# Optimization experiments

Hardware: AMD Instinct MI355X
Metric: run time of the kernel (lower is better)

Reference implementation:

```python
import jax, jax.numpy as jnp
import numpy as np

HIDDEN = 4096
NUM_HEADS = 32
NUM_KV_HEADS = 8
HEAD_DIM = HIDDEN // NUM_HEADS  # 128
ROPE_THETA = 500000.0
WORLD_SIZE = 4  # number of ring blocks (simulated single-device)


def setup_inputs() -> dict:
    key = jax.random.key(0)
    ks = jax.random.split(key, 5)
    B, S = 1, 2048
    wscale = HIDDEN ** -0.5  # keep activations O(1)
    return {
        "hidden_states": jax.random.normal(ks[0], (B, S, HIDDEN), jnp.float32),
        "position_ids": jnp.broadcast_to(jnp.arange(S, dtype=jnp.int32), (B, S)),
        "q_proj": jax.random.normal(ks[1], (NUM_HEADS * HEAD_DIM, HIDDEN), jnp.float32) * wscale,
        "k_proj": jax.random.normal(ks[2], (NUM_KV_HEADS * HEAD_DIM, HIDDEN), jnp.float32) * wscale,
        "v_proj": jax.random.normal(ks[3], (NUM_KV_HEADS * HEAD_DIM, HIDDEN), jnp.float32) * wscale,
        "o_proj": jax.random.normal(ks[4], (HIDDEN, NUM_HEADS * HEAD_DIM), jnp.float32) * wscale,
    }


def _rope_cos_sin(position_ids):
    # LlamaRotaryEmbedding: inv_freq over even dims, emb = cat(freqs, freqs)
    inv_freq = 1.0 / (ROPE_THETA ** (jnp.arange(0, HEAD_DIM, 2, dtype=jnp.float32) / HEAD_DIM))
    freqs = position_ids.astype(jnp.float32)[..., None] * inv_freq  # [B,S,HD/2]
    emb = jnp.concatenate([freqs, freqs], axis=-1)                  # [B,S,HD]
    return jnp.cos(emb), jnp.sin(emb)


def _rotate_half(x):
    x1, x2 = jnp.split(x, 2, axis=-1)
    return jnp.concatenate([-x2, x1], axis=-1)


def _attention_forward(hidden_states, q_proj, k_proj, v_proj, o_proj, position_ids):
    B, S, _ = hidden_states.shape
    # projections (no bias), layout [B, S, H, D] as in the source (view before RoPE)
    q = (hidden_states @ q_proj.T).reshape(B, S, NUM_HEADS, HEAD_DIM)
    k = (hidden_states @ k_proj.T).reshape(B, S, NUM_KV_HEADS, HEAD_DIM)
    v = (hidden_states @ v_proj.T).reshape(B, S, NUM_KV_HEADS, HEAD_DIM)

    cos, sin = _rope_cos_sin(position_ids)        # [B,S,HD]
    c, s = cos[:, :, None, :], sin[:, :, None, :]  # unsqueeze_dim=2
    q = q * c + _rotate_half(q) * s
    k = k * c + _rotate_half(k) * s

    # GQA: expand KV heads to match query heads
    groups = NUM_HEADS // NUM_KV_HEADS
    k = jnp.repeat(k, groups, axis=2)  # [B,S,NH,HD]
    v = jnp.repeat(v, groups, axis=2)

    sm_scale = HEAD_DIM ** -0.5
    blk = S // WORLD_SIZE

    # ring: per-KV-block partial attention (non-causal, as no mask is passed) + LSE
    outs, lses = [], []
    for w in range(WORLD_SIZE):
        kb = k[:, w * blk:(w + 1) * blk]
        vb = v[:, w * blk:(w + 1) * blk]
        scores = jnp.einsum('bqhd,bkhd->bhqk', q, kb) * sm_scale  # [B,NH,S,blk]
        m = jnp.max(scores, axis=-1, keepdims=True)
        p = jnp.exp(scores - m)
        l = jnp.sum(p, axis=-1, keepdims=True)
        outs.append(jnp.einsum('bhqk,bkhd->bqhd', p / l, vb))      # normalized partial out
        lses.append((m + jnp.log(l))[..., 0])                      # [B,NH,S]

    # merge_attentions: weight each block by exp(lse_b - logsumexp(lse))
    lse_all = jnp.stack(lses, axis=0)                 # [W,B,NH,S]
    wgt = jax.nn.softmax(lse_all, axis=0)
    attn = sum(outs[w] * jnp.transpose(wgt[w], (0, 2, 1))[..., None]
               for w in range(WORLD_SIZE))            # [B,S,NH,HD]

    attn = attn.reshape(B, S, NUM_HEADS * HEAD_DIM)
    return attn @ o_proj.T


def reference(hidden_states, position_ids, q_proj, k_proj, v_proj, o_proj):
    return _attention_forward(hidden_states, q_proj, k_proj, v_proj, o_proj, position_ids)
```

## Files before the change

### kernel.cpp

```cpp
#include <hip/hip_runtime.h>
#include <stdint.h>
#include <cmath>

typedef unsigned short u16;
typedef unsigned int u32;
typedef __attribute__((ext_vector_type(8))) __bf16 bf16x8;
typedef __attribute__((ext_vector_type(4))) float f32x4;

#define HIDDEN 4096
#define NH 32
#define NKV 8
#define HD 128
#define S_LEN 2048

__device__ __forceinline__ u16 f2bf(float f) {
    u32 x = __float_as_uint(f);
    x += 0x7fff + ((x >> 16) & 1);
    return (u16)(x >> 16);
}
__device__ __forceinline__ float bf2f(u16 u) {
    return __uint_as_float(((u32)u) << 16);
}
__device__ __forceinline__ float fexp2(float x) {
#if __has_builtin(__builtin_amdgcn_exp2f)
    return __builtin_amdgcn_exp2f(x);
#else
    return __expf(x * 0.6931471805599453f);
#endif
}

typedef __attribute__((address_space(1))) const void gv_t;
typedef __attribute__((address_space(3))) void lv_t;
__device__ __forceinline__ void async16(const u16* g, u16* s) {
    __builtin_amdgcn_global_load_lds((gv_t*)g, (lv_t*)s, 16, 0, 0);
}

#define F4_HS   2097152u
#define F4_WQ   4194304u
#define F4_WKV  1048576u
__global__ void cvt_all(const float* __restrict__ s0, const float* __restrict__ s1,
                        const float* __restrict__ s2, const float* __restrict__ s3,
                        const float* __restrict__ s4, u16* __restrict__ dst) {
    u32 i = blockIdx.x * 256 + threadIdx.x;
    const float* src; u32 off;
    if (i < F4_HS)                              { src = s0; off = 0; }
    else if (i < F4_HS + F4_WQ)                 { src = s1; off = F4_HS; }
    else if (i < F4_HS + F4_WQ + F4_WKV)        { src = s2; off = F4_HS + F4_WQ; }
    else if (i < F4_HS + F4_WQ + 2 * F4_WKV)    { src = s3; off = F4_HS + F4_WQ + F4_WKV; }
    else                                        { src = s4; off = F4_HS + F4_WQ + 2 * F4_WKV; }
    float4 v = ((const float4*)src)[i - off];
    union { u16 u[4]; uint2 w; } pk;
    pk.u[0] = f2bf(v.x); pk.u[1] = f2bf(v.y);
    pk.u[2] = f2bf(v.z); pk.u[3] = f2bf(v.w);
    ((uint2*)dst)[i] = pk.w;
}

#define GEMM_PROLOGUE_AND_MAINLOOP(Aptr, Bptr, Kdim)                                   \
    __shared__ u16 sMem[2][128 * 64];                                                  \
    u16* const sA = sMem[0];                                                           \
    u16* const sB = sMem[1];                                                           \
    const int tid = threadIdx.x;                                                       \
    const int w = tid >> 6, lane = tid & 63;                                           \
    const int l15 = lane & 15, quad = lane >> 4;                                       \
    const int m0 = blockIdx.y * 128, n0 = blockIdx.x * 128;                            \
    const int wm = w & 1, wn = w >> 1;                                                 \
    f32x4 acc[4][4];                                                                   \
    _Pragma("unroll") for (int mi = 0; mi < 4; ++mi)                                   \
    _Pragma("unroll") for (int ni = 0; ni < 4; ++ni)                                   \
    _Pragma("unroll") for (int r = 0; r < 4; ++r) acc[mi][ni][r] = 0.f;                \
    for (int kt = 0; kt < (Kdim); kt += 64) {                                          \
        _Pragma("unroll") for (int i = 0; i < 4; ++i) {                                \
            int c = (i * 4 + w) * 64 + lane;                                           \
            int r = c >> 3, sl = c & 7, g = sl ^ (r & 7);                              \
            async16((Aptr) + (size_t)(m0 + r) * (Kdim) + kt + g * 8, &sA[c * 8]);      \
        }                                                                              \
        _Pragma("unroll") for (int i = 0; i < 4; ++i) {                                \
            int c = (i * 4 + w) * 64 + lane;                                           \
            int r = c >> 3, sl = c & 7, g = sl ^ (r & 7);                              \
            async16((Bptr) + (size_t)(n0 + r) * (Kdim) + kt + g * 8, &sB[c * 8]);      \
        }                                                                              \
        __syncthreads();                                                               \
        _Pragma("unroll") for (int ks = 0; ks < 2; ++ks) {                             \
            bf16x8 af[4], bf[4];                                                       \
            _Pragma("unroll") for (int t = 0; t < 4; ++t) {                            \
                int row = wm * 64 + t * 16 + l15;                                      \
                int sl = (ks * 4 + quad) ^ (row & 7);                                  \
                af[t] = *(const bf16x8*)&sA[row * 64 + sl * 8];                        \
            }                                                                          \
            _Pragma("unroll") for (int t = 0; t < 4; ++t) {                            \
                int row = wn * 64 + t * 16 + l15;                                      \
                int sl = (ks * 4 + quad) ^ (row & 7);                                  \
                bf[t] = *(const bf16x8*)&sB[row * 64 + sl * 8];                        \
            }                                                                          \
            _Pragma("unroll") for (int mi = 0; mi < 4; ++mi)                           \
            _Pragma("unroll") for (int ni = 0; ni < 4; ++ni)                           \
                acc[mi][ni] = __builtin_amdgcn_mfma_f32_16x16x32_bf16(                 \
                    af[mi], bf[ni], acc[mi][ni], 0, 0, 0);                             \
        }                                                                              \
        __syncthreads();                                                               \
    }

__global__ __launch_bounds__(256, 2) void gemm_bt_f32(
    const u16* __restrict__ A, const u16* __restrict__ B, float* __restrict__ C,
    int N, int K)
{
    GEMM_PROLOGUE_AND_MAINLOOP(A, B, K)
#pragma unroll
    for (int mi = 0; mi < 4; ++mi) {
        int row = m0 + wm * 64 + mi * 16 + quad * 4;
#pragma unroll
        for (int ni = 0; ni < 4; ++ni) {
            int col = n0 + wn * 64 + ni * 16 + l15;
#pragma unroll
            for (int r = 0; r < 4; ++r)
                C[(size_t)(row + r) * N + col] = acc[mi][ni][r];
        }
    }
}

__global__ __launch_bounds__(256, 2) void gemm_qkv(
    const u16* __restrict__ A, const u16* __restrict__ B,
    u16* __restrict__ qb, u16* __restrict__ kbuf, u16* __restrict__ vt,
    const float2* __restrict__ tab)
{
    GEMM_PROLOGUE_AND_MAINLOOP(A, B, HIDDEN)
    if (n0 < 4096) {
#pragma unroll
        for (int mi = 0; mi < 4; ++mi) {
            int row = m0 + wm * 64 + mi * 16 + quad * 4;
#pragma unroll
            for (int ni = 0; ni < 4; ++ni) {
                int col = n0 + wn * 64 + ni * 16 + l15;
#pragma unroll
                for (int r = 0; r < 4; ++r)
                    qb[(size_t)(row + r) * HIDDEN + col] = f2bf(acc[mi][ni][r]);
            }
        }
    } else if (n0 < 4096 + 1024) {
        u16* const sT = (u16*)sMem;
        int cb = n0 - 4096;
#pragma unroll
        for (int mi = 0; mi < 4; ++mi)
#pragma unroll
            for (int ni = 0; ni < 4; ++ni) {
                int cl = wn * 64 + ni * 16 + l15;
#pragma unroll
                for (int r = 0; r < 4; ++r) {
                    int rl = wm * 64 + mi * 16 + quad * 4 + r;
                    sT[rl * 128 + cl] = f2bf(acc[mi][ni][r]);
                }
            }
        __syncthreads();
#pragma unroll
        for (int mi = 0; mi < 4; ++mi)
#pragma unroll
            for (int ni = 0; ni < 4; ++ni) {
                int cl = wn * 64 + ni * 16 + l15;
#pragma unroll
                for (int r = 0; r < 4; ++r) {
                    int rl = wm * 64 + mi * 16 + quad * 4 + r;
                    int srow = m0 + rl;
                    float x1 = bf2f(sT[rl * 128 + cl]);
                    float x2 = bf2f(sT[rl * 128 + (cl ^ 64)]);
                    float2 cs = tab[(size_t)srow * 64 + (cl & 63)];
                    float o = (cl < 64) ? (x1 * cs.x - x2 * cs.y)
                                        : (x1 * cs.x + x2 * cs.y);
                    kbuf[(size_t)srow * (NKV * HD) + cb + cl] = f2bf(o);
                }
            }
    } else {
        int cb = n0 - (4096 + 1024);
#pragma unroll
        for (int mi = 0; mi < 4; ++mi) {
            int row = m0 + wm * 64 + mi * 16 + quad * 4;
#pragma unroll
            for (int ni = 0; ni < 4; ++ni) {
                int c = cb + wn * 64 + ni * 16 + l15;
                union { u16 u[4]; uint2 v; } pk;
#pragma unroll
                for (int r = 0; r < 4; ++r) pk.u[r] = f2bf(acc[mi][ni][r]);
                *(uint2*)&vt[(size_t)c * S_LEN + row] = pk.v;
            }
        }
    }
}

struct DTab { double f[64]; };
__global__ void rope_table(const int* __restrict__ pos, float2* __restrict__ tab,
                           DTab dt) {
    int idx = blockIdx.x * 256 + threadIdx.x;
    int d = idx & 63, s = idx >> 6;
    double fr = (double)pos[s] * dt.f[d];
    double sd, cd;
    sincos(fr, &sd, &cd);
    tab[idx] = make_float2((float)cd, (float)sd);
}

__global__ __launch_bounds__(256, 2) void attn_kernel(
    const u16* __restrict__ Q, const u16* __restrict__ Kb,
    const u16* __restrict__ Vt, u16* __restrict__ O,
    const float2* __restrict__ tab, float qscale)
{
    __shared__ u16 sK[2][64 * 128];
    __shared__ u16 sV[2][128 * 64];

    const int tid = threadIdx.x;
    const int w = tid >> 6, lane = tid & 63;
    const int l15 = lane & 15, quad = lane >> 4;
    const int h = blockIdx.y, q0 = blockIdx.x * 128;
    const int hk = h >> 2;

    bf16x8 qf[2][4];
#pragma unroll
    for (int mt = 0; mt < 2; ++mt) {
        int srow = q0 + w * 32 + mt * 16 + l15;
        const u16* qrow = Q + (size_t)srow * HIDDEN + h * HD;
        bf16x8 raw[4];
#pragma unroll
        for (int ks = 0; ks < 4; ++ks)
            raw[ks] = *(const bf16x8*)(qrow + ks * 32 + quad * 8);
#pragma unroll
        for (int a = 0; a < 2; ++a) {
            const float2* tp = &tab[(size_t)srow * 64 + a * 32 + quad * 8];
#pragma unroll
            for (int j = 0; j < 8; ++j) {
                float c = tp[j].x * qscale, sn = tp[j].y * qscale;
                float x1 = (float)raw[a][j], x2 = (float)raw[a + 2][j];
                qf[mt][a][j]     = (__bf16)(x1 * c - x2 * sn);
                qf[mt][a + 2][j] = (__bf16)(x2 * c + x1 * sn);
            }
        }
    }

    f32x4 oc[8][2];
#pragma unroll
    for (int dt = 0; dt < 8; ++dt)
#pragma unroll
        for (int nt = 0; nt < 2; ++nt)
#pragma unroll
            for (int r = 0; r < 4; ++r) oc[dt][nt][r] = 0.f;
    float m_r[2], l_r[2];
#pragma unroll
    for (int mt = 0; mt < 2; ++mt) { m_r[mt] = -1e30f; l_r[mt] = 0.f; }

    auto stageK = [&](int k0, u16* dst) {
#pragma unroll
        for (int i = 0; i < 4; ++i) {
            int c = i * 256 + tid;
            int r = c >> 4, sl = c & 15, g = sl ^ (r & 15);
            async16(Kb + (size_t)(k0 + r) * (NKV * HD) + hk * HD + g * 8, &dst[c * 8]);
        }
    };
    auto stageV = [&](int k0, u16* dst) {
#pragma unroll
        for (int i = 0; i < 4; ++i) {
            int c = i * 256 + tid;
            int r = c >> 3, sl = c & 7, g = sl ^ (r & 7);
            async16(Vt + (size_t)(hk * HD + r) * S_LEN + k0 + g * 8, &dst[c * 8]);
        }
    };

    stageK(0, sK[0]);
    stageV(0, sV[0]);
    __syncthreads();

    int cur = 0;
    for (int kbi = 0; kbi < 32; ++kbi) {
        if (kbi < 31) {
            stageK((kbi + 1) * 64, sK[cur ^ 1]);
            stageV((kbi + 1) * 64, sV[cur ^ 1]);
        }
        const u16* sKc = sK[cur];
        const u16* sVc = sV[cur];

        f32x4 sa[4][2];
#pragma unroll
        for (int nt = 0; nt < 4; ++nt)
#pragma unroll
            for (int mt = 0; mt < 2; ++mt)
#pragma unroll
                for (int r = 0; r < 4; ++r) sa[nt][mt][r] = 0.f;
#pragma unroll
        for (int ks = 0; ks < 4; ++ks) {
            bf16x8 kf[4];
#pragma unroll
            for (int nt = 0; nt < 4; ++nt) {
                int row = nt * 16 + l15;
                int sl = (ks * 4 + quad) ^ (row & 15);
                kf[nt] = *(const bf16x8*)&sKc[row * 128 + sl * 8];
            }
#pragma unroll
            for (int nt = 0; nt < 4; ++nt)
#pragma unroll
                for (int mt = 0; mt < 2; ++mt)
                    sa[nt][mt] = __builtin_amdgcn_mfma_f32_16x16x32_bf16(
                        kf[nt], qf[mt][ks], sa[nt][mt], 0, 0, 0);
        }

        float mxv[2];
        bool grow = false;
#pragma unroll
        for (int mt = 0; mt < 2; ++mt) {
            float mx = sa[0][mt][0];
#pragma unroll
            for (int nt = 0; nt < 4; ++nt)
#pragma unroll
                for (int r = 0; r < 4; ++r)
                    if (nt || r) mx = fmaxf(mx, sa[nt][mt][r]);
            mx = fmaxf(mx, __shfl_xor(mx, 16));
            mx = fmaxf(mx, __shfl_xor(mx, 32));
            mxv[mt] = mx;
            grow = grow || (mx > m_r[mt] + 8.f);
        }
        const int dorescale = __any((int)grow);
        if (dorescale) {
            float al[2];
#pragma unroll
            for (int mt = 0; mt < 2; ++mt) {
                float mnew = fmaxf(m_r[mt], mxv[mt]);
                al[mt] = fexp2(m_r[mt] - mnew);
                m_r[mt] = mnew;
                l_r[mt] *= al[mt];
            }
#pragma unroll
            for (int dt = 0; dt < 8; ++dt)
#pragma unroll
                for (int r = 0; r < 4; ++r) { oc[dt][0][r] *= al[0]; oc[dt][1][r] *= al[1]; }
        }

        bf16x8 pf[2][2];
#pragma unroll
        for (int mt = 0; mt < 2; ++mt) {
            float mm = m_r[mt];
            float lsum = 0.f;
#pragma unroll
            for (int ntk = 0; ntk < 4; ++ntk) {
                float p0 = fexp2(sa[ntk][mt][0] - mm);
                float p1 = fexp2(sa[ntk][mt][1] - mm);
                float p2 = fexp2(sa[ntk][mt][2] - mm);
                float p3 = fexp2(sa[ntk][mt][3] - mm);
                lsum += (p0 + p1) + (p2 + p3);
                const int kx = ntk >> 1, e = (ntk & 1) * 4;
                pf[kx][mt][e + 0] = (__bf16)p0;
                pf[kx][mt][e + 1] = (__bf16)p1;
                pf[kx][mt][e + 2] = (__bf16)p2;
                pf[kx][mt][e + 3] = (__bf16)p3;
            }
            l_r[mt] += lsum;
        }

#pragma unroll
        for (int ks = 0; ks < 2; ++ks) {
#pragma unroll
            for (int dt = 0; dt < 8; ++dt) {
                int row = dt * 16 + l15;
                int g1 = (ks * 4 + (quad >> 1)) ^ (row & 7);
                int base = row * 64 + (quad & 1) * 4;
                union { uint2 u2[2]; bf16x8 v; } vfu;
                vfu.u2[0] = *(const uint2*)&sVc[base + g1 * 8];
                vfu.u2[1] = *(const uint2*)&sVc[base + (g1 ^ 2) * 8];
#pragma unroll
                for (int nt = 0; nt < 2; ++nt)
                    oc[dt][nt] = __builtin_amdgcn_mfma_f32_16x16x32_bf16(
                        vfu.v, pf[ks][nt], oc[dt][nt], 0, 0, 0);
            }
        }

        __syncthreads();
        cur ^= 1;
    }

    float il[2];
#pragma unroll
    for (int mt = 0; mt < 2; ++mt) {
        float ls = l_r[mt];
        ls += __shfl_xor(ls, 16);
        ls += __shfl_xor(ls, 32);
        il[mt] = 1.f / ls;
    }
#pragma unroll
    for (int nt = 0; nt < 2; ++nt)
#pragma unroll
        for (int dt = 0; dt < 8; ++dt) {
            union { u16 u[4]; uint2 v; } pk;
#pragma unroll
            for (int r = 0; r < 4; ++r) pk.u[r] = f2bf(oc[dt][nt][r] * il[nt]);
            *(uint2*)(O + (size_t)(q0 + w * 32 + nt * 16 + l15) * HIDDEN
                        + h * HD + dt * 16 + quad * 4) = pk.v;
        }
}

extern "C" void kernel_launch(void* const* d_in, const int* in_sizes, int n_in,
                              void* d_out, int out_size, void* d_ws, size_t ws_size,
                              hipStream_t stream) {
    const float* hs = (const float*)d_in[0];
    const int* pos  = (const int*)d_in[1];
    const float* wq = (const float*)d_in[2];
    const float* wk = (const float*)d_in[3];
    const float* wv = (const float*)d_in[4];
    const float* wo = (const float*)d_in[5];
    float* out = (float*)d_out;

    u16* ws    = (u16*)d_ws;
    u16* hid16 = ws;
    u16* wq16  = hid16 + (size_t)S_LEN * HIDDEN;
    u16* wk16  = wq16 + (size_t)HIDDEN * HIDDEN;
    u16* wv16  = wk16 + (size_t)NKV * HD * HIDDEN;
    u16* wo16  = wv16 + (size_t)NKV * HD * HIDDEN;
    u16* qb    = wo16 + (size_t)HIDDEN * HIDDEN;
    u16* kb    = qb + (size_t)S_LEN * HIDDEN;
    u16* vt    = kb + (size_t)S_LEN * NKV * HD;
    u16* at    = vt + (size_t)S_LEN * NKV * HD;
    float2* tab = (float2*)(at + (size_t)S_LEN * HIDDEN);

    dim3 blk(256);

    cvt_all<<<dim3(12582912u / 256), blk, 0, stream>>>(hs, wq, wk, wv, wo, hid16);

    DTab dt;
    for (int i = 0; i < 64; ++i) dt.f[i] = pow(500000.0, -(double)i / 64.0);
    rope_table<<<dim3(S_LEN * 64 / 256), blk, 0, stream>>>(pos, tab, dt);

    gemm_qkv<<<dim3((HIDDEN + 2 * NKV * HD) / 128, S_LEN / 128), blk, 0, stream>>>(
        hid16, wq16, qb, kb, vt, tab);

    const float qscale = 0.08838834764831845f * 1.4426950408889634f;
    attn_kernel<<<dim3(S_LEN / 128, NH), dim3(256), 0, stream>>>(
        qb, kb, vt, at, tab, qscale);

    gemm_bt_f32<<<dim3(HIDDEN / 128, S_LEN / 128), blk, 0, stream>>>(
        at, wo16, out, HIDDEN, HIDDEN);
}
```

Measured before the change: 456.0 us.

## Fuse fp32-to-bf16 conversion into GEMM tile loads, drop cvt_all pass

Removes the separate conversion kernel that cast hidden states and all weights to bf16 in workspace. The QKV and output-projection GEMMs now stage fp32 tiles straight into LDS with async loads and convert to bf16 when reading MFMA fragments. This saves one full read-write pass over about 50M floats, but doubles the bytes each GEMM tile loads and doubles LDS use (64KB per block for QKV), which may lower occupancy and adds conversion work inside the inner loop.

```diff
diff --git a/kernel.cpp b/kernel.cpp
--- a/kernel.cpp
+++ b/kernel.cpp
@@ -34,96 +34,89 @@
 __device__ __forceinline__ void async16(const u16* g, u16* s) {
     __builtin_amdgcn_global_load_lds((gv_t*)g, (lv_t*)s, 16, 0, 0);
 }
-
-#define F4_HS   2097152u
-#define F4_WQ   4194304u
-#define F4_WKV  1048576u
-__global__ void cvt_all(const float* __restrict__ s0, const float* __restrict__ s1,
-                        const float* __restrict__ s2, const float* __restrict__ s3,
-                        const float* __restrict__ s4, u16* __restrict__ dst) {
-    u32 i = blockIdx.x * 256 + threadIdx.x;
-    const float* src; u32 off;
-    if (i < F4_HS)                              { src = s0; off = 0; }
-    else if (i < F4_HS + F4_WQ)                 { src = s1; off = F4_HS; }
-    else if (i < F4_HS + F4_WQ + F4_WKV)        { src = s2; off = F4_HS + F4_WQ; }
-    else if (i < F4_HS + F4_WQ + 2 * F4_WKV)    { src = s3; off = F4_HS + F4_WQ + F4_WKV; }
-    else                                        { src = s4; off = F4_HS + F4_WQ + 2 * F4_WKV; }
-    float4 v = ((const float4*)src)[i - off];
-    union { u16 u[4]; uint2 w; } pk;
-    pk.u[0] = f2bf(v.x); pk.u[1] = f2bf(v.y);
-    pk.u[2] = f2bf(v.z); pk.u[3] = f2bf(v.w);
-    ((uint2*)dst)[i] = pk.w;
-}
-
-#define GEMM_PROLOGUE_AND_MAINLOOP(Aptr, Bptr, Kdim)                                   \
-    __shared__ u16 sMem[2][128 * 64];                                                  \
-    u16* const sA = sMem[0];                                                           \
-    u16* const sB = sMem[1];                                                           \
-    const int tid = threadIdx.x;                                                       \
-    const int w = tid >> 6, lane = tid & 63;                                           \
-    const int l15 = lane & 15, quad = lane >> 4;                                       \
-    const int m0 = blockIdx.y * 128, n0 = blockIdx.x * 128;                            \
-    const int wm = w & 1, wn = w >> 1;                                                 \
-    f32x4 acc[4][4];                                                                   \
-    _Pragma("unroll") for (int mi = 0; mi < 4; ++mi)                                   \
-    _Pragma("unroll") for (int ni = 0; ni < 4; ++ni)                                   \
-    _Pragma("unroll") for (int r = 0; r < 4; ++r) acc[mi][ni][r] = 0.f;                \
-    for (int kt = 0; kt < (Kdim); kt += 64) {                                          \
-        _Pragma("unroll") for (int i = 0; i < 4; ++i) {                                \
-            int c = (i * 4 + w) * 64 + lane;                                           \
-            int r = c >> 3, sl = c & 7, g = sl ^ (r & 7);                              \
-            async16((Aptr) + (size_t)(m0 + r) * (Kdim) + kt + g * 8, &sA[c * 8]);      \
-        }                                                                              \
-        _Pragma("unroll") for (int i = 0; i < 4; ++i) {                                \
-            int c = (i * 4 + w) * 64 + lane;                                           \
-            int r = c >> 3, sl = c & 7, g = sl ^ (r & 7);                              \
-            async16((Bptr) + (size_t)(n0 + r) * (Kdim) + kt + g * 8, &sB[c * 8]);      \
-        }                                                                              \
-        __syncthreads();                                                               \
-        _Pragma("unroll") for (int ks = 0; ks < 2; ++ks) {                             \
-            bf16x8 af[4], bf[4];                                                       \
-            _Pragma("unroll") for (int t = 0; t < 4; ++t) {                            \
-                int row = wm * 64 + t * 16 + l15;                                      \
-                int sl = (ks * 4 + quad) ^ (row & 7);                                  \
-                af[t] = *(const bf16x8*)&sA[row * 64 + sl * 8];                        \
-            }                                                                          \
-            _Pragma("unroll") for (int t = 0; t < 4; ++t) {                            \
-                int row = wn * 64 + t * 16 + l15;                                      \
-                int sl = (ks * 4 + quad) ^ (row & 7);                                  \
-                bf[t] = *(const bf16x8*)&sB[row * 64 + sl * 8];                        \
-            }                                                                          \
-            _Pragma("unroll") for (int mi = 0; mi < 4; ++mi)                           \
-            _Pragma("unroll") for (int ni = 0; ni < 4; ++ni)                           \
-                acc[mi][ni] = __builtin_amdgcn_mfma_f32_16x16x32_bf16(                 \
-                    af[mi], bf[ni], acc[mi][ni], 0, 0, 0);                             \
-        }                                                                              \
-        __syncthreads();                                                               \
-    }
-
-__global__ __launch_bounds__(256, 2) void gemm_bt_f32(
-    const u16* __restrict__ A, const u16* __restrict__ B, float* __restrict__ C,
-    int N, int K)
-{
-    GEMM_PROLOGUE_AND_MAINLOOP(A, B, K)
-#pragma unroll
-    for (int mi = 0; mi < 4; ++mi) {
-        int row = m0 + wm * 64 + mi * 16 + quad * 4;
-#pragma unroll
-        for (int ni = 0; ni < 4; ++ni) {
-            int col = n0 + wn * 64 + ni * 16 + l15;
-#pragma unroll
-            for (int r = 0; r < 4; ++r)
-                C[(size_t)(row + r) * N + col] = acc[mi][ni][r];
-        }
-    }
+__device__ __forceinline__ void async16f(const float* g, float* s) {
+    __builtin_amdgcn_global_load_lds((gv_t*)g, (lv_t*)s, 16, 0, 0);
+}
+
+#define STAGE_F32(SRC, LDK, DST)                                                       \
+    _Pragma("unroll") for (int i = 0; i < 8; ++i) {                                    \
+        int c = i * 256 + tid;                                                         \
+        int r = c >> 4, sl = c & 15, g = sl ^ (r & 15);                                \
+        async16f((SRC) + (size_t)r * (LDK) + g * 4, &(DST)[c * 4]);                    \
+    }
+
+__device__ __forceinline__ bf16x8 read_f32_frag(const float* sF, int row, int ks, int quad) {
+    int ch = ks * 8 + quad * 2, rm = row & 15;
+    f32x4 a = *(const f32x4*)&sF[row * 64 + ((ch ^ rm) << 2)];
+    f32x4 b = *(const f32x4*)&sF[row * 64 + (((ch + 1) ^ rm) << 2)];
+    bf16x8 f;
+#pragma unroll
+    for (int j = 0; j < 4; ++j) { f[j] = (__bf16)a[j]; f[4 + j] = (__bf16)b[j]; }
+    return f;
+}
+
+struct DTab { double f[64]; };
+__global__ void rope_table(const int* __restrict__ pos, float2* __restrict__ tab,
+                           DTab dt) {
+    int idx = blockIdx.x * 256 + threadIdx.x;
+    int d = idx & 63, s = idx >> 6;
+    double fr = (double)pos[s] * dt.f[d];
+    double sd, cd;
+    sincos(fr, &sd, &cd);
+    tab[idx] = make_float2((float)cd, (float)sd);
 }
 
 __global__ __launch_bounds__(256, 2) void gemm_qkv(
-    const u16* __restrict__ A, const u16* __restrict__ B,
+    const float* __restrict__ A, const float* __restrict__ Wq,
+    const float* __restrict__ Wk, const float* __restrict__ Wv,
     u16* __restrict__ qb, u16* __restrict__ kbuf, u16* __restrict__ vt,
     const float2* __restrict__ tab)
 {
-    GEMM_PROLOGUE_AND_MAINLOOP(A, B, HIDDEN)
+    __shared__ __align__(16) float sMemF[2][128 * 64];
+    float* const sA = sMemF[0];
+    float* const sB = sMemF[1];
+    const int tid = threadIdx.x;
+    const int w = tid >> 6, lane = tid & 63;
+    const int l15 = lane & 15, quad = lane >> 4;
+    const int m0 = blockIdx.y * 128, n0 = blockIdx.x * 128;
+    const int wm = w & 1, wn = w >> 1;
+
+    const float* Bp; int nb;
+    if (n0 < 4096)      { Bp = Wq; nb = n0; }
+    else if (n0 < 5120) { Bp = Wk; nb = n0 - 4096; }
+    else                { Bp = Wv; nb = n0 - 5120; }
+
+    f32x4 acc[4][4];
+#pragma unroll
+    for (int mi = 0; mi < 4; ++mi)
+#pragma unroll
+        for (int ni = 0; ni < 4; ++ni)
+#pragma unroll
+            for (int r = 0; r < 4; ++r) acc[mi][ni][r] = 0.f;
+
+    for (int kt = 0; kt < HIDDEN; kt += 64) {
+        STAGE_F32(A + (size_t)m0 * HIDDEN + kt, HIDDEN, sA)
+        STAGE_F32(Bp + (size_t)nb * HIDDEN + kt, HIDDEN, sB)
+        __syncthreads();
+#pragma unroll
+        for (int ks = 0; ks < 2; ++ks) {
+            bf16x8 af[4], bf[4];
+#pragma unroll
+            for (int t = 0; t < 4; ++t)
+                af[t] = read_f32_frag(sA, wm * 64 + t * 16 + l15, ks, quad);
+#pragma unroll
+            for (int t = 0; t < 4; ++t)
+                bf[t] = read_f32_frag(sB, wn * 64 + t * 16 + l15, ks, quad);
+#pragma unroll
+            for (int mi = 0; mi < 4; ++mi)
+#pragma unroll
+                for (int ni = 0; ni < 4; ++ni)
+                    acc[mi][ni] = __builtin_amdgcn_mfma_f32_16x16x32_bf16(
+                        af[mi], bf[ni], acc[mi][ni], 0, 0, 0);
+        }
+        __syncthreads();
+    }
+
     if (n0 < 4096) {
 #pragma unroll
         for (int mi = 0; mi < 4; ++mi) {
@@ -136,8 +129,8 @@
                     qb[(size_t)(row + r) * HIDDEN + col] = f2bf(acc[mi][ni][r]);
             }
         }
-    } else if (n0 < 4096 + 1024) {
-        u16* const sT = (u16*)sMem;
+    } else if (n0 < 5120) {
+        u16* const sT = (u16*)sMemF;
         int cb = n0 - 4096;
 #pragma unroll
         for (int mi = 0; mi < 4; ++mi)
@@ -169,7 +162,7 @@
                 }
             }
     } else {
-        int cb = n0 - (4096 + 1024);
+        int cb = n0 - 5120;
 #pragma unroll
         for (int mi = 0; mi < 4; ++mi) {
             int row = m0 + wm * 64 + mi * 16 + quad * 4;
@@ -185,15 +178,67 @@
     }
 }
 
-struct DTab { double f[64]; };
-__global__ void rope_table(const int* __restrict__ pos, float2* __restrict__ tab,
-                           DTab dt) {
-    int idx = blockIdx.x * 256 + threadIdx.x;
-    int d = idx & 63, s = idx >> 6;
-    double fr = (double)pos[s] * dt.f[d];
-    double sd, cd;
-    sincos(fr, &sd, &cd);
-    tab[idx] = make_float2((float)cd, (float)sd);
+__global__ __launch_bounds__(256, 2) void gemm_bt_f32(
+    const u16* __restrict__ A, const float* __restrict__ B, float* __restrict__ C,
+    int N, int K)
+{
+    __shared__ __align__(16) u16 sA[128 * 64];
+    __shared__ __align__(16) float sB[128 * 64];
+    const int tid = threadIdx.x;
+    const int w = tid >> 6, lane = tid & 63;
+    const int l15 = lane & 15, quad = lane >> 4;
+    const int m0 = blockIdx.y * 128, n0 = blockIdx.x * 128;
+    const int wm = w & 1, wn = w >> 1;
+
+    f32x4 acc[4][4];
+#pragma unroll
+    for (int mi = 0; mi < 4; ++mi)
+#pragma unroll
+        for (int ni = 0; ni < 4; ++ni)
+#pragma unroll
+            for (int r = 0; r < 4; ++r) acc[mi][ni][r] = 0.f;
+
+    for (int kt = 0; kt < K; kt += 64) {
+#pragma unroll
+        for (int i = 0; i < 4; ++i) {
+            int c = (i * 4 + w) * 64 + lane;
+            int r = c >> 3, sl = c & 7, g = sl ^ (r & 7);
+            async16(A + (size_t)(m0 + r) * K + kt + g * 8, &sA[c * 8]);
+        }
+        STAGE_F32(B + (size_t)n0 * K + kt, K, sB)
+        __syncthreads();
+#pragma unroll
+        for (int ks = 0; ks < 2; ++ks) {
+            bf16x8 af[4], bf[4];
+#pragma unroll
+            for (int t = 0; t < 4; ++t) {
+                int row = wm * 64 + t * 16 + l15;
+                int sl = (ks * 4 + quad) ^ (row & 7);
+                af[t] = *(const bf16x8*)&sA[row * 64 + sl * 8];
+            }
+#pragma unroll
+            for (int t = 0; t < 4; ++t)
+                bf[t] = read_f32_frag(sB, wn * 64 + t * 16 + l15, ks, quad);
+#pragma unroll
+            for (int mi = 0; mi < 4; ++mi)
+#pragma unroll
+                for (int ni = 0; ni < 4; ++ni)
+                    acc[mi][ni] = __builtin_amdgcn_mfma_f32_16x16x32_bf16(
+                        af[mi], bf[ni], acc[mi][ni], 0, 0, 0);
+        }
+        __syncthreads();
+    }
+#pragma unroll
+    for (int mi = 0; mi < 4; ++mi) {
+        int row = m0 + wm * 64 + mi * 16 + quad * 4;
+#pragma unroll
+        for (int ni = 0; ni < 4; ++ni) {
+            int col = n0 + wn * 64 + ni * 16 + l15;
+#pragma unroll
+            for (int r = 0; r < 4; ++r)
+                C[(size_t)(row + r) * N + col] = acc[mi][ni][r];
+        }
+    }
 }
 
 __global__ __launch_bounds__(256, 2) void attn_kernel(
@@ -402,12 +447,7 @@
     float* out = (float*)d_out;
 
     u16* ws    = (u16*)d_ws;
-    u16* hid16 = ws;
-    u16* wq16  = hid16 + (size_t)S_LEN * HIDDEN;
-    u16* wk16  = wq16 + (size_t)HIDDEN * HIDDEN;
-    u16* wv16  = wk16 + (size_t)NKV * HD * HIDDEN;
-    u16* wo16  = wv16 + (size_t)NKV * HD * HIDDEN;
-    u16* qb    = wo16 + (size_t)HIDDEN * HIDDEN;
+    u16* qb    = ws;
     u16* kb    = qb + (size_t)S_LEN * HIDDEN;
     u16* vt    = kb + (size_t)S_LEN * NKV * HD;
     u16* at    = vt + (size_t)S_LEN * NKV * HD;
@@ -415,19 +455,17 @@
 
     dim3 blk(256);
 
-    cvt_all<<<dim3(12582912u / 256), blk, 0, stream>>>(hs, wq, wk, wv, wo, hid16);
-
     DTab dt;
     for (int i = 0; i < 64; ++i) dt.f[i] = pow(500000.0, -(double)i / 64.0);
     rope_table<<<dim3(S_LEN * 64 / 256), blk, 0, stream>>>(pos, tab, dt);
 
     gemm_qkv<<<dim3((HIDDEN + 2 * NKV * HD) / 128, S_LEN / 128), blk, 0, stream>>>(
-        hid16, wq16, qb, kb, vt, tab);
+        hs, wq, wk, wv, qb, kb, vt, tab);
 
     const float qscale = 0.08838834764831845f * 1.4426950408889634f;
     attn_kernel<<<dim3(S_LEN / 128, NH), dim3(256), 0, stream>>>(
         qb, kb, vt, at, tab, qscale);
 
     gemm_bt_f32<<<dim3(HIDDEN / 128, S_LEN / 128), blk, 0, stream>>>(
-        at, wo16, out, HIDDEN, HIDDEN);
-}
+        at, wo, out, HIDDEN, HIDDEN);
+}
```

Result: slower. 576.2 us (+26.4%).
